# Optimization experiments

Measured on AMD Instinct MI355X. Metric: run time of the kernel, lower is better.

## Reference

```python
import jax, jax.numpy as jnp
import numpy as np
from math import log2, floor

B, N, DIM = 2, 2048, 2048
HEADS, DIM_HEAD, FF_MULT = 16, 128, 4
RMS_EPS = 1e-8


def _get_slopes(heads):
    def pow2_slopes(n):
        start = 2 ** (-2 ** (-(log2(n) - 3)))
        return [start * start ** i for i in range(n)]
    if log2(heads).is_integer():
        return pow2_slopes(heads)
    closest = 2 ** floor(log2(heads))
    return pow2_slopes(closest) + pow2_slopes(2 * closest)[0::2][: heads - closest]


def setup_inputs() -> dict:
    key = jax.random.key(0)
    ks = jax.random.split(key, 5)
    std = 0.02
    return {
        "x": jax.random.normal(ks[0], (B, N, DIM), dtype=jnp.float32),
        "g": jnp.ones((DIM,), dtype=jnp.float32),
        "w_qkv": jax.random.normal(ks[1], (DIM, DIM + DIM_HEAD), dtype=jnp.float32) * std,
        "w_attn_out": jax.random.normal(ks[2], (DIM, DIM), dtype=jnp.float32) * std,
        "w_ff1": jax.random.normal(ks[3], (DIM, 2 * FF_MULT * DIM), dtype=jnp.float32) * std,
        "w_ff2": jax.random.normal(ks[4], (FF_MULT * DIM, DIM), dtype=jnp.float32) * std,
    }


def reference(x, g, w_qkv, w_attn_out, w_ff1, w_ff2):
    b, n, dim = x.shape
    # RMSNorm: x / clamp(||x|| * dim^-0.5, eps) * g
    norm = jnp.linalg.norm(x, axis=-1, keepdims=True) * (dim ** -0.5)
    xn = x / jnp.maximum(norm, RMS_EPS) * g

    # Parallel SwiGLU FFN branch (shares normed input with attention)
    h = xn @ w_ff1                       # [b, n, 2*ff_mult*dim]
    val, gate = jnp.split(h, 2, axis=-1)
    ff_out = (jax.nn.silu(gate) * val) @ w_ff2  # [b, n, dim]

    # Multi-query attention: single dim_head-wide kv shared as K and V
    qkv = xn @ w_qkv                     # [b, n, dim + dim_head]
    q, kv = qkv[..., :dim], qkv[..., dim:]
    q = q.reshape(b, n, HEADS, DIM_HEAD) * (DIM_HEAD ** -0.5)
    sim = jnp.einsum('bihd,bjd->bhij', q, kv)  # [b, h, n, n]

    # ALiBi bias: -|j - i| * slope_h
    slopes = jnp.asarray(_get_slopes(HEADS), dtype=sim.dtype)[:, None, None]
    pos = jnp.arange(n)
    bias = -jnp.abs(pos[None, None, :] - pos[None, :, None]).astype(sim.dtype) * slopes
    sim = sim + bias

    # Causal mask (strict upper triangle masked)
    causal = jnp.triu(jnp.ones((n, n), dtype=bool), 1)
    neg = jnp.asarray(jnp.finfo(sim.dtype).max, sim.dtype)
    sim = jnp.where(causal, -neg, sim)

    attn = jax.nn.softmax(sim, axis=-1)
    out = jnp.einsum('bhij,bjd->bhid', attn, kv)     # [b, h, n, dim_head]
    out = out.transpose(0, 2, 1, 3).reshape(b, n, dim)
    return out @ w_attn_out + ff_out
```

## Files before the change

### kernel.cpp

```cpp
#include <hip/hip_runtime.h>
#include <stdint.h>

typedef unsigned short u16;
typedef __attribute__((ext_vector_type(8))) short bf16x8;
typedef __attribute__((ext_vector_type(4))) float f32x4;
typedef __attribute__((ext_vector_type(8))) unsigned short us8;
typedef __attribute__((ext_vector_type(4))) float fvec4;

#define BATCH 2
#define SEQ   2048
#define DIMM  2048
#define NH    16
#define DH    128
#define ROWS  (BATCH*SEQ)
#define QKVN  (DIMM + DH)
#define FFH   8192
#define LOG2E 1.44269504088896340736f

static __device__ __forceinline__ u16 f2bf(float x) {
  union { float f; uint32_t u; } v; v.f = x;
  uint32_t r = (v.u + 0x7fffu + ((v.u >> 16) & 1u)) >> 16;
  return (u16)r;
}

static __device__ __forceinline__ float fast_exp2(float x) {
  float r; asm("v_exp_f32 %0, %1" : "=v"(r) : "v"(x)); return r;
}

static __device__ __forceinline__ void gld_lds16(const void* g, void* l) {
  __builtin_amdgcn_global_load_lds(
      (const __attribute__((address_space(1))) uint32_t*)g,
      (__attribute__((address_space(3))) uint32_t*)l, 16, 0, 0);
}

__global__ __launch_bounds__(256)
void rmsnorm_k(const float* __restrict__ x, const float* __restrict__ g, u16* __restrict__ xn) {
  const int row = blockIdx.x;
  const float* xr = x + (size_t)row * DIMM;
  const int off = threadIdx.x * 8;
  fvec4 a = *(const fvec4*)(xr + off);
  fvec4 b = *(const fvec4*)(xr + off + 4);
  float ss = a[0]*a[0]+a[1]*a[1]+a[2]*a[2]+a[3]*a[3]
           + b[0]*b[0]+b[1]*b[1]+b[2]*b[2]+b[3]*b[3];
  #pragma unroll
  for (int m = 32; m >= 1; m >>= 1) ss += __shfl_xor(ss, m);
  __shared__ float red[4];
  if ((threadIdx.x & 63) == 0) red[threadIdx.x >> 6] = ss;
  __syncthreads();
  float tot = red[0] + red[1] + red[2] + red[3];
  float inv = 1.0f / fmaxf(sqrtf(tot * (1.0f / DIMM)), 1e-8f);
  fvec4 ga = *(const fvec4*)(g + off);
  fvec4 gb = *(const fvec4*)(g + off + 4);
  us8 o;
  #pragma unroll
  for (int i = 0; i < 4; i++) { o[i] = f2bf(a[i]*inv*ga[i]); o[4+i] = f2bf(b[i]*inv*gb[i]); }
  *(us8*)(xn + (size_t)row * DIMM + off) = o;
}

template<typename TIN>
__global__ __launch_bounds__(256)
void transpose_to_bf16(const TIN* __restrict__ in, u16* __restrict__ out, int R, int C) {
  __shared__ u16 tile[64 * 65];
  const int r0 = blockIdx.y * 64, c0 = blockIdx.x * 64;
  const int tr = threadIdx.x >> 2;
  const int tc = (threadIdx.x & 3) * 16;
  const TIN* ip = in + (size_t)(r0 + tr) * C + c0 + tc;
  u16 tmp[16];
  #pragma unroll
  for (int i = 0; i < 16; i++) {
    if constexpr (sizeof(TIN) == 4) tmp[i] = f2bf(((const float*)ip)[i]);
    else                            tmp[i] = ((const u16*)ip)[i];
  }
  #pragma unroll
  for (int i = 0; i < 16; i++) tile[tr * 65 + tc + i] = tmp[i];
  __syncthreads();
  const int oc  = c0 + tr;
  const int orr = (threadIdx.x & 3) * 16;
  us8 v0, v1;
  #pragma unroll
  for (int i = 0; i < 8; i++) v0[i] = tile[(orr + i) * 65 + tr];
  #pragma unroll
  for (int i = 0; i < 8; i++) v1[i] = tile[(orr + 8 + i) * 65 + tr];
  u16* op = out + (size_t)oc * R + r0 + orr;
  *(us8*)op = v0;
  *(us8*)(op + 8) = v1;
}

template<int MODE>
__global__ __launch_bounds__(256, 2)
void gemm_bf16(const u16* __restrict__ A, const u16* __restrict__ BT, int K,
               float* __restrict__ outF, u16* __restrict__ outQ, u16* __restrict__ outKV,
               const float* __restrict__ tmpF) {
  __shared__ __align__(16) u16 lA[128 * 32];
  __shared__ __align__(16) u16 lB[128 * 32];
  const int tid = threadIdx.x;
  const int wave = tid >> 6, lane = tid & 63;
  const int lid = lane & 15, quad = lane >> 4;
  const int wm = wave >> 1, wn = wave & 1;
  const int row0 = blockIdx.y * 128;
  const int col0 = blockIdx.x * 128;
  f32x4 acc[4][4];
  #pragma unroll
  for (int i = 0; i < 4; i++)
    #pragma unroll
    for (int j = 0; j < 4; j++) { acc[i][j][0]=0.f; acc[i][j][1]=0.f; acc[i][j][2]=0.f; acc[i][j][3]=0.f; }

  const int rA0 = wave * 32;
  const int rsub = lane >> 2;
  const int cl = lane & 3;

  for (int k0 = 0; k0 < K; k0 += 32) {
    #pragma unroll
    for (int h2 = 0; h2 < 2; ++h2) {
      int rloc = rA0 + h2 * 16 + rsub;
      int gc = cl ^ ((rloc >> 1) & 3);
      gld_lds16(A  + (size_t)(row0 + rloc) * K + k0 + gc * 8, lA + (rA0 + h2 * 16) * 32);
      gld_lds16(BT + (size_t)(col0 + rloc) * K + k0 + gc * 8, lB + (rA0 + h2 * 16) * 32);
    }
    __syncthreads();
    bf16x8 af[4], bfr[4];
    #pragma unroll
    for (int i = 0; i < 4; i++) {
      int r  = wm * 64 + i * 16 + lid;
      af[i]  = *(const bf16x8*)(lA + r * 32 + (quad ^ ((r >> 1) & 3)) * 8);
      int rb = wn * 64 + i * 16 + lid;
      bfr[i] = *(const bf16x8*)(lB + rb * 32 + (quad ^ ((rb >> 1) & 3)) * 8);
    }
    #pragma unroll
    for (int im = 0; im < 4; im++)
      #pragma unroll
      for (int in = 0; in < 4; in++)
        acc[im][in] = __builtin_amdgcn_mfma_f32_16x16x32_bf16(af[im], bfr[in], acc[im][in], 0, 0, 0);
    __syncthreads();
  }

  #pragma unroll
  for (int im = 0; im < 4; im++)
    #pragma unroll
    for (int in = 0; in < 4; in++) {
      int col = col0 + wn * 64 + in * 16 + lid;
      int rbase = row0 + wm * 64 + im * 16 + quad * 4;
      #pragma unroll
      for (int rg = 0; rg < 4; rg++) {
        float v = acc[im][in][rg];
        int row = rbase + rg;
        if constexpr (MODE == 0) {
          if (col < DIMM) outQ[(size_t)row * DIMM + col] = f2bf(v);
          else            outKV[(size_t)row * DH + (col - DIMM)] = f2bf(v);
        } else if constexpr (MODE == 2) {
          outF[(size_t)row * DIMM + col] = v;
        } else {
          size_t idx = (size_t)row * DIMM + col;
          outF[idx] += v + tmpF[idx];
        }
      }
    }
}

static __device__ __forceinline__ void stage_half(const u16* __restrict__ src, u16* dst,
                                                  int K, int sr, int sgc, int wave) {
  gld_lds16(src + (size_t)sr * K + sgc,       dst + wave * 1024);
  gld_lds16(src + (size_t)(sr + 8) * K + sgc, dst + wave * 1024 + 512);
}

static __device__ __forceinline__ void lda4(bf16x8 (&dst)[4][2], const u16* sAb,
                                            int mh, int wm, int lid, int c0) {
  #pragma unroll
  for (int i = 0; i < 4; ++i) {
    const u16* p = sAb + (mh * 128 + wm * 64 + i * 16 + lid) * 64;
    dst[i][0] = *(const bf16x8*)(p + c0);
    dst[i][1] = *(const bf16x8*)(p + (c0 ^ 32));
  }
}

static __device__ __forceinline__ void ldb2(bf16x8 (&dst)[2][2], const u16* sBb,
                                            int nh, int wn, int lid, int c0) {
  #pragma unroll
  for (int n = 0; n < 2; ++n) {
    const u16* p = sBb + (nh * 128 + wn * 32 + n * 16 + lid) * 64;
    dst[n][0] = *(const bf16x8*)(p + c0);
    dst[n][1] = *(const bf16x8*)(p + (c0 ^ 32));
  }
}

static __device__ __forceinline__ void quad16(f32x4 (&acc)[8][4], const bf16x8 (&af)[4][2],
                                              const bf16x8 (&bf)[2][2], int mh, int nh) {
  __builtin_amdgcn_s_setprio(1);
  #pragma unroll
  for (int i = 0; i < 4; ++i)
    #pragma unroll
    for (int n = 0; n < 2; ++n) {
      f32x4 c = acc[mh * 4 + i][nh * 2 + n];
      c = __builtin_amdgcn_mfma_f32_16x16x32_bf16(af[i][0], bf[n][0], c, 0, 0, 0);
      c = __builtin_amdgcn_mfma_f32_16x16x32_bf16(af[i][1], bf[n][1], c, 0, 0, 0);
      acc[mh * 4 + i][nh * 2 + n] = c;
    }
  __builtin_amdgcn_s_setprio(0);
}

#define VMW(n) asm volatile("s_waitcnt vmcnt(" #n ")" ::: "memory")
#define BAR8() __builtin_amdgcn_s_barrier()

#define EIGHT_PHASE_LOOP(NITER)                                               \
  {                                                                           \
    STAGE_A(0,0,0); STAGE_B(0,0,0); STAGE_B(0,1,0); STAGE_A(0,1,0);           \
    STAGE_A(1,0,1); STAGE_B(1,0,1); STAGE_B(1,1,1);                           \
    VMW(6);                                                                   \
    BAR8();                                                                   \
    lda4(af, sA[0], 0, wm, lid, c0);                              \
    ldb2(bW, sB[0], 0, wn, lid, c0);                              \
    for (int I = 0; I < (NITER); ++I) {                                       \
      const bool more = (I + 1 < (NITER));                                    \
      const int kt1 = 2*I+1, kt2 = 2*I+2, kt3 = 2*I+3;                        \
                                         \
      STAGE_A(1,1,kt1);                                                       \
      BAR8();                                                                 \
      quad16(acc, af, bW, 0, 0);                                              \
      ldb2(bX, sB[0], 1, wn, lid, c0);                                        \
      VMW(8);                                                                 \
      BAR8();                                                                 \
                                            \
      if (more) STAGE_A(0,0,kt2);                                             \
      BAR8();                                                                 \
      quad16(acc, af, bX, 0, 1);                                              \
      lda4(af, sA[0], 1, wm, lid, c0);                                        \
      BAR8();                                                                 \
                                                              \
      if (more) STAGE_B(0,0,kt2);                                             \
      BAR8();                                                                 \
      quad16(acc, af, bX, 1, 1);                                              \
      if (more) { VMW(8); } else { VMW(4); }                                  \
      BAR8();                                                                 \
                                    \
      if (more) STAGE_B(0,1,kt2);                                             \
      BAR8();                                                                 \
      quad16(acc, af, bW, 1, 0);                                              \
      ldb2(bW, sB[1], 0, wn, lid, c0);                                        \
      lda4(af, sA[1], 0, wm, lid, c0);                                        \
      if (more) { VMW(8); } else { VMW(2); }                                  \
      BAR8();                                                                 \
                                         \
      if (more) STAGE_A(0,1,kt2);                                             \
      BAR8();                                                                 \
      quad16(acc, af, bW, 0, 0);                                              \
      ldb2(bX, sB[1], 1, wn, lid, c0);                                        \
      if (more) { VMW(8); } else { VMW(0); }                                  \
      BAR8();                                                                 \
                                            \
      if (more) STAGE_A(1,0,kt3);                                             \
      BAR8();                                                                 \
      quad16(acc, af, bX, 0, 1);                                              \
      lda4(af, sA[1], 1, wm, lid, c0);                                        \
      BAR8();                                                                 \
                                                              \
      if (more) STAGE_B(1,0,kt3);                                             \
      BAR8();                                                                 \
      quad16(acc, af, bX, 1, 1);                                              \
      if (more) { VMW(8); }                                                   \
      BAR8();                                                                 \
                                  \
      if (more) STAGE_B(1,1,kt3);                                             \
      BAR8();                                                                 \
      quad16(acc, af, bW, 1, 0);                                              \
      if (more) {                                                             \
        ldb2(bW, sB[0], 0, wn, lid, c0);                                      \
        lda4(af, sA[0], 0, wm, lid, c0);                                      \
        VMW(8);                                                               \
      }                                                                       \
      BAR8();                                                                 \
    }                                                                         \
  }

__global__ __launch_bounds__(512, 2)
void gemm_ff1_swiglu_8p(const u16* __restrict__ A, const u16* __restrict__ BT,
                        u16* __restrict__ FF) {
  __shared__ __align__(16) u16 sA[2][256 * 64];
  __shared__ __align__(16) u16 sB[2][256 * 64];
  const int tid = threadIdx.x;
  const int wave = tid >> 6, lane = tid & 63;
  const int lid = lane & 15, quad = lane >> 4;
  const int wm = wave >> 2, wn = wave & 3;
  const int K = DIMM;

  int orig = blockIdx.y * 64 + blockIdx.x;
  int swz = (orig & 7) * 128 + (orig >> 3);
  const int row0 = (swz >> 6) * 256;
  const int n0 = (swz & 63) * 128;

  const int sr  = wave * 16 + (lane >> 3);
  const int sgc = (((lane & 7) ^ (lane >> 3)) << 3);
  const int c0  = ((quad ^ (lid & 7)) << 3);

  f32x4 acc[8][4];
  #pragma unroll
  for (int i = 0; i < 8; ++i)
    #pragma unroll
    for (int j = 0; j < 4; ++j) { acc[i][j][0]=0.f; acc[i][j][1]=0.f; acc[i][j][2]=0.f; acc[i][j][3]=0.f; }
  bf16x8 af[4][2], bW[2][2], bX[2][2];

  #define STAGE_A(b, h, kt) stage_half(A  + (size_t)(row0 + (h)*128) * K + (kt)*64, &sA[b][(h)*8192], K, sr, sgc, wave)
  #define STAGE_B(b, h, kt) stage_half(BT + (size_t)((h) ? (FFH + n0) : n0) * K + (kt)*64, &sB[b][(h)*8192], K, sr, sgc, wave)

  EIGHT_PHASE_LOOP(K / 128)

  #undef STAGE_A
  #undef STAGE_B

  #pragma unroll
  for (int mi = 0; mi < 8; ++mi) {
    const int row = row0 + (mi >> 2) * 128 + wm * 64 + (mi & 3) * 16 + quad * 4;
    #pragma unroll
    for (int n = 0; n < 2; ++n) {
      const int col = n0 + wn * 32 + n * 16 + lid;
      #pragma unroll
      for (int rg = 0; rg < 4; ++rg) {
        float vv = acc[mi][n][rg];
        float gg = acc[mi][2 + n][rg];
        float sig = 1.0f / (1.0f + fast_exp2(-gg * LOG2E));
        FF[(size_t)(row + rg) * FFH + col] = f2bf(vv * gg * sig);
      }
    }
  }
}

__global__ __launch_bounds__(512, 2)
void gemm_ff2_8p(const u16* __restrict__ A, const u16* __restrict__ BT,
                 float* __restrict__ out0, float* __restrict__ out1) {
  __shared__ __align__(16) u16 sA[2][256 * 64];
  __shared__ __align__(16) u16 sB[2][256 * 64];
  const int tid = threadIdx.x;
  const int wave = tid >> 6, lane = tid & 63;
  const int lid = lane & 15, quad = lane >> 4;
  const int wm = wave >> 2, wn = wave & 3;
  const int K = FFH;

  int orig = (blockIdx.z * 16 + blockIdx.y) * 8 + blockIdx.x;
  int swz = (orig & 7) * 32 + (orig >> 3);
  const int n0   = (swz & 7) * 256;
  const int ks   = (swz >> 3) & 1;
  const int row0 = (swz >> 4) * 256;

  const u16* Ab = A  + ks * 4096;
  const u16* Bb = BT + ks * 4096;

  const int sr  = wave * 16 + (lane >> 3);
  const int sgc = (((lane & 7) ^ (lane >> 3)) << 3);
  const int c0  = ((quad ^ (lid & 7)) << 3);

  f32x4 acc[8][4];
  #pragma unroll
  for (int i = 0; i < 8; ++i)
    #pragma unroll
    for (int j = 0; j < 4; ++j) { acc[i][j][0]=0.f; acc[i][j][1]=0.f; acc[i][j][2]=0.f; acc[i][j][3]=0.f; }
  bf16x8 af[4][2], bW[2][2], bX[2][2];

  #define STAGE_A(b, h, kt) stage_half(Ab + (size_t)(row0 + (h)*128) * K + (kt)*64, &sA[b][(h)*8192], K, sr, sgc, wave)
  #define STAGE_B(b, h, kt) stage_half(Bb + (size_t)(n0 + (h)*128) * K + (kt)*64,  &sB[b][(h)*8192], K, sr, sgc, wave)

  EIGHT_PHASE_LOOP(32)

  #undef STAGE_A
  #undef STAGE_B

  float* dst = ks ? out1 : out0;
  #pragma unroll
  for (int mi = 0; mi < 8; ++mi) {
    const int row = row0 + (mi >> 2) * 128 + wm * 64 + (mi & 3) * 16 + quad * 4;
    #pragma unroll
    for (int j = 0; j < 4; ++j) {
      const int col = n0 + (j >> 1) * 128 + wn * 32 + (j & 1) * 16 + lid;
      #pragma unroll
      for (int rg = 0; rg < 4; ++rg)
        dst[(size_t)(row + rg) * DIMM + col] = acc[mi][j][rg];
    }
  }
}

__global__ __launch_bounds__(256, 1)
void attn_k2(const u16* __restrict__ qws, const u16* __restrict__ kvws,
             const u16* __restrict__ kvt, u16* __restrict__ attnws) {
  __shared__ __align__(16) u16 kvls[128 * 128];
  __shared__ __align__(16) u16 kvtls[128 * 128];
  __shared__ __align__(16) u16 plds[4][32][136];
  const int tid = threadIdx.x;
  const int wave = tid >> 6, lane = tid & 63;
  const int lid = lane & 15, quad = lane >> 4;
  const int hb = blockIdx.y;
  const int h = hb & (NH - 1), b = hb >> 4;
  const int pair = blockIdx.x;
  const float slope2 = fast_exp2(-0.5f * (float)(h + 1)) * LOG2E;
  const float scale2 = 0.08838834764831845f * LOG2E;
  const float NEG = -__builtin_inff();

  const u16* kvb  = kvws + (size_t)b * SEQ * DH;
  const u16* kvtb = kvt  + (size_t)b * DH * SEQ;

  #pragma unroll 1
  for (int tt = 0; tt < 2; tt++) {
    const int T = tt ? (15 - pair) : pair;
    const int rw = T * 128 + wave * 32;

    bf16x8 qf[2][4];
    #pragma unroll
    for (int ig = 0; ig < 2; ig++)
      #pragma unroll
      for (int ks = 0; ks < 4; ks++)
        qf[ig][ks] = *(const bf16x8*)(qws + (size_t)(b * SEQ + rw + ig * 16 + lid) * DIMM
                                       + h * DH + ks * 32 + quad * 8);
    float srow2[2][4];
    #pragma unroll
    for (int ig = 0; ig < 2; ig++)
      #pragma unroll
      for (int rg = 0; rg < 4; rg++)
        srow2[ig][rg] = slope2 * (float)(rw + ig * 16 + quad * 4 + rg);

    f32x4 o[2][8];
    #pragma unroll
    for (int ig = 0; ig < 2; ig++)
      #pragma unroll
      for (int nd = 0; nd < 8; nd++) { o[ig][nd][0]=0.f; o[ig][nd][1]=0.f; o[ig][nd][2]=0.f; o[ig][nd][3]=0.f; }
    float m2[2][4], l[2][4];
    #pragma unroll
    for (int ig = 0; ig < 2; ig++)
      #pragma unroll
      for (int rg = 0; rg < 4; rg++) { m2[ig][rg] = NEG; l[ig][rg] = 0.f; }

    const int njt = T + 1;
    #pragma unroll 1
    for (int jt = 0; jt < njt; jt++) {
      const int j0 = jt * 128;
      __syncthreads();
      {
        const int c = lane & 15;
        const int r4 = lane >> 4;
        #pragma unroll
        for (int it = 0; it < 8; it++) {
          const int r = wave * 32 + it * 4 + r4;
          const int gc = c ^ (r & 15);
          gld_lds16(kvb  + (size_t)(j0 + r) * DH + gc * 8,        kvls  + (wave * 32 + it * 4) * 128);
          gld_lds16(kvtb + (size_t)r * SEQ + j0 + gc * 8,         kvtls + (wave * 32 + it * 4) * 128);
        }
      }
      __syncthreads();

      const int rhi = rw + 31;
      const int nbmax = min(8, ((rhi - j0) >> 4) + 1);
      const int ks2max = (nbmax + 1) >> 1;

      float pvv[2][8][4];
      float mt[2][4];
      #pragma unroll
      for (int ig = 0; ig < 2; ig++)
        #pragma unroll
        for (int rg = 0; rg < 4; rg++) mt[ig][rg] = NEG;

      #pragma unroll
      for (int nb = 0; nb < 8; nb++) {
        if (nb < nbmax) {
          bf16x8 bk[4];
          #pragma unroll
          for (int ks = 0; ks < 4; ks++)
            bk[ks] = *(const bf16x8*)(kvls + (nb * 16 + lid) * 128 + (((ks * 4 + quad) ^ lid) << 3));
          f32x4 s0, s1;
          s0[0]=0.f;s0[1]=0.f;s0[2]=0.f;s0[3]=0.f;
          s1[0]=0.f;s1[1]=0.f;s1[2]=0.f;s1[3]=0.f;
          #pragma unroll
          for (int ks = 0; ks < 4; ks++) {
            s0 = __builtin_amdgcn_mfma_f32_16x16x32_bf16(qf[0][ks], bk[ks], s0, 0, 0, 0);
            s1 = __builtin_amdgcn_mfma_f32_16x16x32_bf16(qf[1][ks], bk[ks], s1, 0, 0, 0);
          }
          const int jl = j0 + nb * 16 + lid;
          const float sj = slope2 * (float)jl;
          #pragma unroll
          for (int rg = 0; rg < 4; rg++) {
            const int row0r = rw + quad * 4 + rg;
            float e0 = fmaf(s0[rg], scale2, sj) - srow2[0][rg];
            e0 = (jl <= row0r) ? e0 : NEG;
            pvv[0][nb][rg] = e0;
            mt[0][rg] = fmaxf(mt[0][rg], e0);
            float e1 = fmaf(s1[rg], scale2, sj) - srow2[1][rg];
            e1 = (jl <= row0r + 16) ? e1 : NEG;
            pvv[1][nb][rg] = e1;
            mt[1][rg] = fmaxf(mt[1][rg], e1);
          }
        }
      }

      float alpha[2][4];
      #pragma unroll
      for (int ig = 0; ig < 2; ig++)
        #pragma unroll
        for (int rg = 0; rg < 4; rg++) {
          float m = mt[ig][rg];
          m = fmaxf(m, __shfl_xor(m, 1));
          m = fmaxf(m, __shfl_xor(m, 2));
          m = fmaxf(m, __shfl_xor(m, 4));
          m = fmaxf(m, __shfl_xor(m, 8));
          float mn = fmaxf(m2[ig][rg], m);
          alpha[ig][rg] = fast_exp2(m2[ig][rg] - mn);
          m2[ig][rg] = mn;
        }

      float rs[2][4];
      #pragma unroll
      for (int ig = 0; ig < 2; ig++)
        #pragma unroll
        for (int rg = 0; rg < 4; rg++) rs[ig][rg] = 0.f;
      #pragma unroll
      for (int nb = 0; nb < 8; nb++) {
        if (nb < nbmax) {
          #pragma unroll
          for (int ig = 0; ig < 2; ig++)
            #pragma unroll
            for (int rg = 0; rg < 4; rg++) {
              float p = fast_exp2(pvv[ig][nb][rg] - m2[ig][rg]);
              rs[ig][rg] += p;
              plds[wave][ig * 16 + quad * 4 + rg][nb * 16 + lid] = f2bf(p);
            }
        }
      }
      if (nbmax & 1) {
        #pragma unroll
        for (int ig = 0; ig < 2; ig++)
          #pragma unroll
          for (int rg = 0; rg < 4; rg++)
            plds[wave][ig * 16 + quad * 4 + rg][nbmax * 16 + lid] = 0;
      }

      #pragma unroll
      for (int ig = 0; ig < 2; ig++)
        #pragma unroll
        for (int rg = 0; rg < 4; rg++) {
          float r = rs[ig][rg];
          r += __shfl_xor(r, 1);
          r += __shfl_xor(r, 2);
          r += __shfl_xor(r, 4);
          r += __shfl_xor(r, 8);
          l[ig][rg] = l[ig][rg] * alpha[ig][rg] + r;
        }
      #pragma unroll
      for (int ig = 0; ig < 2; ig++)
        #pragma unroll
        for (int nd = 0; nd < 8; nd++)
          #pragma unroll
          for (int rg = 0; rg < 4; rg++) o[ig][nd][rg] *= alpha[ig][rg];

      asm volatile("s_waitcnt lgkmcnt(0)" ::: "memory");
      #pragma unroll
      for (int ks2 = 0; ks2 < 4; ks2++) {
        if (ks2 < ks2max) {
          bf16x8 pa0 = *(const bf16x8*)&plds[wave][lid][ks2 * 32 + quad * 8];
          bf16x8 pa1 = *(const bf16x8*)&plds[wave][16 + lid][ks2 * 32 + quad * 8];
          #pragma unroll
          for (int nd = 0; nd < 8; nd++) {
            bf16x8 bv = *(const bf16x8*)(kvtls + (nd * 16 + lid) * 128 + (((ks2 * 4 + quad) ^ lid) << 3));
            o[0][nd] = __builtin_amdgcn_mfma_f32_16x16x32_bf16(pa0, bv, o[0][nd], 0, 0, 0);
            o[1][nd] = __builtin_amdgcn_mfma_f32_16x16x32_bf16(pa1, bv, o[1][nd], 0, 0, 0);
          }
        }
      }
    }

    #pragma unroll
    for (int ig = 0; ig < 2; ig++) {
      float inv[4];
      #pragma unroll
      for (int rg = 0; rg < 4; rg++) inv[rg] = 1.0f / l[ig][rg];
      #pragma unroll
      for (int nd = 0; nd < 8; nd++)
        #pragma unroll
        for (int rg = 0; rg < 4; rg++) {
          int row = rw + ig * 16 + quad * 4 + rg;
          attnws[(size_t)(b * SEQ + row) * DIMM + h * DH + nd * 16 + lid] =
              f2bf(o[ig][nd][rg] * inv[rg]);
        }
    }
  }
}

extern "C" void kernel_launch(void* const* d_in, const int* in_sizes, int n_in,
                              void* d_out, int out_size, void* d_ws, size_t ws_size,
                              hipStream_t stream) {
  (void)in_sizes; (void)n_in; (void)out_size; (void)ws_size;
  const float* x     = (const float*)d_in[0];
  const float* g     = (const float*)d_in[1];
  const float* w_qkv = (const float*)d_in[2];
  const float* w_ao  = (const float*)d_in[3];
  const float* w_ff1 = (const float*)d_in[4];
  const float* w_ff2 = (const float*)d_in[5];
  float* out = (float*)d_out;

  u16* ws = (u16*)d_ws;
  u16* xn     = ws;
  u16* wTqkv  = xn     + 8388608;
  u16* wTattn = wTqkv  + 4456448;
  u16* wTff1  = wTattn + 4194304;
  u16* wTff2  = wTff1  + 33554432;
  u16* ffin   = wTff2  + 16777216;
  u16* qws    = ffin   + 33554432;
  u16* kvws   = qws    + 8388608;
  u16* kvtws  = kvws   + 524288;
  u16* attnws = kvtws  + 524288;
  float* tmpf = (float*)wTff1;

  transpose_to_bf16<float><<<dim3(QKVN/64, DIMM/64), 256, 0, stream>>>(w_qkv, wTqkv, DIMM, QKVN);
  transpose_to_bf16<float><<<dim3(DIMM/64, DIMM/64), 256, 0, stream>>>(w_ao, wTattn, DIMM, DIMM);
  transpose_to_bf16<float><<<dim3((2*FFH)/64, DIMM/64), 256, 0, stream>>>(w_ff1, wTff1, DIMM, 2*FFH);
  transpose_to_bf16<float><<<dim3(DIMM/64, FFH/64), 256, 0, stream>>>(w_ff2, wTff2, FFH, DIMM);

  rmsnorm_k<<<ROWS, 256, 0, stream>>>(x, g, xn);

  gemm_bf16<0><<<dim3(QKVN/128, ROWS/128), 256, 0, stream>>>(xn, wTqkv, DIMM, nullptr, qws, kvws, nullptr);

  transpose_to_bf16<u16><<<dim3(DH/64, SEQ/64), 256, 0, stream>>>(kvws, kvtws, SEQ, DH);
  transpose_to_bf16<u16><<<dim3(DH/64, SEQ/64), 256, 0, stream>>>(kvws + (size_t)SEQ*DH, kvtws + (size_t)DH*SEQ, SEQ, DH);

  attn_k2<<<dim3(8, NH*BATCH), 256, 0, stream>>>(qws, kvws, kvtws, attnws);

  gemm_ff1_swiglu_8p<<<dim3(FFH/128, ROWS/256), 512, 0, stream>>>(xn, wTff1, ffin);
  gemm_ff2_8p<<<dim3(8, 16, 2), 512, 0, stream>>>(ffin, wTff2, out, tmpf);

  gemm_bf16<3><<<dim3(DIMM/128, ROWS/128), 256, 0, stream>>>(attnws, wTattn, DIMM, out, nullptr, nullptr, tmpf);
}
```

Before: 924.6 us.

## Shrink attention tiles to 64 rows and double grid for higher occupancy

Reworks the flash-attention kernel to process 64 query rows per block (16 per wave) against 64-column KV tiles, halving LDS use and allowing two blocks per CU. The grid doubles so more blocks cover the GPU and latency can be hidden across blocks. In exchange each wave reuses loaded K fragments across fewer MFMAs, KV tiles are reloaded from global memory twice as often, and block-level syncs per unit of work increase.

```diff
diff --git a/kernel.cpp b/kernel.cpp
--- a/kernel.cpp
+++ b/kernel.cpp
@@ -376,12 +376,12 @@
   }
 }
 
-__global__ __launch_bounds__(256, 1)
-void attn_k2(const u16* __restrict__ qws, const u16* __restrict__ kvws,
+__global__ __launch_bounds__(256, 2)
+void attn_k3(const u16* __restrict__ qws, const u16* __restrict__ kvws,
              const u16* __restrict__ kvt, u16* __restrict__ attnws) {
-  __shared__ __align__(16) u16 kvls[128 * 128];
-  __shared__ __align__(16) u16 kvtls[128 * 128];
-  __shared__ __align__(16) u16 plds[4][32][136];
+  __shared__ __align__(16) u16 kvls[64 * 128];
+  __shared__ __align__(16) u16 kvtls[128 * 64];
+  __shared__ __align__(16) u16 plds[4][16][72];
   const int tid = threadIdx.x;
   const int wave = tid >> 6, lane = tid & 63;
   const int lid = lane & 15, quad = lane >> 4;
@@ -397,184 +397,152 @@
 
   #pragma unroll 1
   for (int tt = 0; tt < 2; tt++) {
-    const int T = tt ? (15 - pair) : pair;
-    const int rw = T * 128 + wave * 32;
-
-    bf16x8 qf[2][4];
-    #pragma unroll
-    for (int ig = 0; ig < 2; ig++)
-      #pragma unroll
-      for (int ks = 0; ks < 4; ks++)
-        qf[ig][ks] = *(const bf16x8*)(qws + (size_t)(b * SEQ + rw + ig * 16 + lid) * DIMM
-                                       + h * DH + ks * 32 + quad * 8);
-    float srow2[2][4];
-    #pragma unroll
-    for (int ig = 0; ig < 2; ig++)
-      #pragma unroll
-      for (int rg = 0; rg < 4; rg++)
-        srow2[ig][rg] = slope2 * (float)(rw + ig * 16 + quad * 4 + rg);
-
-    f32x4 o[2][8];
-    #pragma unroll
-    for (int ig = 0; ig < 2; ig++)
-      #pragma unroll
-      for (int nd = 0; nd < 8; nd++) { o[ig][nd][0]=0.f; o[ig][nd][1]=0.f; o[ig][nd][2]=0.f; o[ig][nd][3]=0.f; }
-    float m2[2][4], l[2][4];
-    #pragma unroll
-    for (int ig = 0; ig < 2; ig++)
-      #pragma unroll
-      for (int rg = 0; rg < 4; rg++) { m2[ig][rg] = NEG; l[ig][rg] = 0.f; }
-
-    const int njt = T + 1;
+    const int TT = tt ? (31 - pair) : pair;
+    const int rw = TT * 64 + wave * 16;
+
+    bf16x8 qf[4];
+    #pragma unroll
+    for (int ks = 0; ks < 4; ks++)
+      qf[ks] = *(const bf16x8*)(qws + (size_t)(b * SEQ + rw + lid) * DIMM
+                                 + h * DH + ks * 32 + quad * 8);
+    float srow[4];
+    #pragma unroll
+    for (int rg = 0; rg < 4; rg++)
+      srow[rg] = slope2 * (float)(rw + quad * 4 + rg);
+
+    f32x4 o[8];
+    #pragma unroll
+    for (int nd = 0; nd < 8; nd++) { o[nd][0]=0.f; o[nd][1]=0.f; o[nd][2]=0.f; o[nd][3]=0.f; }
+    float m2[4], l[4];
+    #pragma unroll
+    for (int rg = 0; rg < 4; rg++) { m2[rg] = NEG; l[rg] = 0.f; }
+
+    const int njt = TT + 1;
     #pragma unroll 1
     for (int jt = 0; jt < njt; jt++) {
-      const int j0 = jt * 128;
+      const int j0 = jt * 64;
       __syncthreads();
       {
-        const int c = lane & 15;
-        const int r4 = lane >> 4;
+        const int c16 = lane & 15, r16 = lane >> 4;
+        const int c8  = lane & 7,  r8  = lane >> 3;
         #pragma unroll
-        for (int it = 0; it < 8; it++) {
-          const int r = wave * 32 + it * 4 + r4;
-          const int gc = c ^ (r & 15);
-          gld_lds16(kvb  + (size_t)(j0 + r) * DH + gc * 8,        kvls  + (wave * 32 + it * 4) * 128);
-          gld_lds16(kvtb + (size_t)r * SEQ + j0 + gc * 8,         kvtls + (wave * 32 + it * 4) * 128);
+        for (int it = 0; it < 4; it++) {
+          const int r  = wave * 16 + it * 4 + r16;
+          const int gc = c16 ^ (r & 15);
+          gld_lds16(kvb + (size_t)(j0 + r) * DH + gc * 8, kvls + (wave * 16 + it * 4) * 128);
+          const int r2  = wave * 32 + it * 8 + r8;
+          const int gc2 = c8 ^ (r2 & 7);
+          gld_lds16(kvtb + (size_t)r2 * SEQ + j0 + gc2 * 8, kvtls + (wave * 32 + it * 8) * 64);
         }
       }
       __syncthreads();
 
-      const int rhi = rw + 31;
-      const int nbmax = min(8, ((rhi - j0) >> 4) + 1);
+      const int nbmax = min(4, ((rw + 15 - j0) >> 4) + 1);
       const int ks2max = (nbmax + 1) >> 1;
 
-      float pvv[2][8][4];
-      float mt[2][4];
-      #pragma unroll
-      for (int ig = 0; ig < 2; ig++)
-        #pragma unroll
-        for (int rg = 0; rg < 4; rg++) mt[ig][rg] = NEG;
-
-      #pragma unroll
-      for (int nb = 0; nb < 8; nb++) {
+      float pvv[4][4];
+      float mt[4];
+      #pragma unroll
+      for (int rg = 0; rg < 4; rg++) mt[rg] = NEG;
+
+      #pragma unroll
+      for (int nb = 0; nb < 4; nb++) {
         if (nb < nbmax) {
           bf16x8 bk[4];
           #pragma unroll
           for (int ks = 0; ks < 4; ks++)
             bk[ks] = *(const bf16x8*)(kvls + (nb * 16 + lid) * 128 + (((ks * 4 + quad) ^ lid) << 3));
-          f32x4 s0, s1;
-          s0[0]=0.f;s0[1]=0.f;s0[2]=0.f;s0[3]=0.f;
-          s1[0]=0.f;s1[1]=0.f;s1[2]=0.f;s1[3]=0.f;
+          f32x4 s;
+          s[0]=0.f; s[1]=0.f; s[2]=0.f; s[3]=0.f;
           #pragma unroll
-          for (int ks = 0; ks < 4; ks++) {
-            s0 = __builtin_amdgcn_mfma_f32_16x16x32_bf16(qf[0][ks], bk[ks], s0, 0, 0, 0);
-            s1 = __builtin_amdgcn_mfma_f32_16x16x32_bf16(qf[1][ks], bk[ks], s1, 0, 0, 0);
-          }
+          for (int ks = 0; ks < 4; ks++)
+            s = __builtin_amdgcn_mfma_f32_16x16x32_bf16(qf[ks], bk[ks], s, 0, 0, 0);
           const int jl = j0 + nb * 16 + lid;
           const float sj = slope2 * (float)jl;
           #pragma unroll
           for (int rg = 0; rg < 4; rg++) {
             const int row0r = rw + quad * 4 + rg;
-            float e0 = fmaf(s0[rg], scale2, sj) - srow2[0][rg];
-            e0 = (jl <= row0r) ? e0 : NEG;
-            pvv[0][nb][rg] = e0;
-            mt[0][rg] = fmaxf(mt[0][rg], e0);
-            float e1 = fmaf(s1[rg], scale2, sj) - srow2[1][rg];
-            e1 = (jl <= row0r + 16) ? e1 : NEG;
-            pvv[1][nb][rg] = e1;
-            mt[1][rg] = fmaxf(mt[1][rg], e1);
+            float e = fmaf(s[rg], scale2, sj) - srow[rg];
+            e = (jl <= row0r) ? e : NEG;
+            pvv[nb][rg] = e;
+            mt[rg] = fmaxf(mt[rg], e);
           }
         }
       }
 
-      float alpha[2][4];
-      #pragma unroll
-      for (int ig = 0; ig < 2; ig++)
-        #pragma unroll
-        for (int rg = 0; rg < 4; rg++) {
-          float m = mt[ig][rg];
-          m = fmaxf(m, __shfl_xor(m, 1));
-          m = fmaxf(m, __shfl_xor(m, 2));
-          m = fmaxf(m, __shfl_xor(m, 4));
-          m = fmaxf(m, __shfl_xor(m, 8));
-          float mn = fmaxf(m2[ig][rg], m);
-          alpha[ig][rg] = fast_exp2(m2[ig][rg] - mn);
-          m2[ig][rg] = mn;
-        }
-
-      float rs[2][4];
-      #pragma unroll
-      for (int ig = 0; ig < 2; ig++)
-        #pragma unroll
-        for (int rg = 0; rg < 4; rg++) rs[ig][rg] = 0.f;
-      #pragma unroll
-      for (int nb = 0; nb < 8; nb++) {
+      float alpha[4];
+      #pragma unroll
+      for (int rg = 0; rg < 4; rg++) {
+        float m = mt[rg];
+        m = fmaxf(m, __shfl_xor(m, 1));
+        m = fmaxf(m, __shfl_xor(m, 2));
+        m = fmaxf(m, __shfl_xor(m, 4));
+        m = fmaxf(m, __shfl_xor(m, 8));
+        float mn = fmaxf(m2[rg], m);
+        alpha[rg] = fast_exp2(m2[rg] - mn);
+        m2[rg] = mn;
+      }
+
+      float rs[4];
+      #pragma unroll
+      for (int rg = 0; rg < 4; rg++) rs[rg] = 0.f;
+      #pragma unroll
+      for (int nb = 0; nb < 4; nb++) {
         if (nb < nbmax) {
           #pragma unroll
-          for (int ig = 0; ig < 2; ig++)
-            #pragma unroll
-            for (int rg = 0; rg < 4; rg++) {
-              float p = fast_exp2(pvv[ig][nb][rg] - m2[ig][rg]);
-              rs[ig][rg] += p;
-              plds[wave][ig * 16 + quad * 4 + rg][nb * 16 + lid] = f2bf(p);
-            }
+          for (int rg = 0; rg < 4; rg++) {
+            float p = fast_exp2(pvv[nb][rg] - m2[rg]);
+            rs[rg] += p;
+            plds[wave][quad * 4 + rg][nb * 16 + lid] = f2bf(p);
+          }
         }
       }
       if (nbmax & 1) {
         #pragma unroll
-        for (int ig = 0; ig < 2; ig++)
-          #pragma unroll
-          for (int rg = 0; rg < 4; rg++)
-            plds[wave][ig * 16 + quad * 4 + rg][nbmax * 16 + lid] = 0;
-      }
-
-      #pragma unroll
-      for (int ig = 0; ig < 2; ig++)
+        for (int rg = 0; rg < 4; rg++)
+          plds[wave][quad * 4 + rg][nbmax * 16 + lid] = 0;
+      }
+
+      #pragma unroll
+      for (int rg = 0; rg < 4; rg++) {
+        float r = rs[rg];
+        r += __shfl_xor(r, 1);
+        r += __shfl_xor(r, 2);
+        r += __shfl_xor(r, 4);
+        r += __shfl_xor(r, 8);
+        l[rg] = l[rg] * alpha[rg] + r;
+      }
+      #pragma unroll
+      for (int nd = 0; nd < 8; nd++)
         #pragma unroll
-        for (int rg = 0; rg < 4; rg++) {
-          float r = rs[ig][rg];
-          r += __shfl_xor(r, 1);
-          r += __shfl_xor(r, 2);
-          r += __shfl_xor(r, 4);
-          r += __shfl_xor(r, 8);
-          l[ig][rg] = l[ig][rg] * alpha[ig][rg] + r;
-        }
-      #pragma unroll
-      for (int ig = 0; ig < 2; ig++)
-        #pragma unroll
-        for (int nd = 0; nd < 8; nd++)
-          #pragma unroll
-          for (int rg = 0; rg < 4; rg++) o[ig][nd][rg] *= alpha[ig][rg];
+        for (int rg = 0; rg < 4; rg++) o[nd][rg] *= alpha[rg];
 
       asm volatile("s_waitcnt lgkmcnt(0)" ::: "memory");
       #pragma unroll
-      for (int ks2 = 0; ks2 < 4; ks2++) {
+      for (int ks2 = 0; ks2 < 2; ks2++) {
         if (ks2 < ks2max) {
-          bf16x8 pa0 = *(const bf16x8*)&plds[wave][lid][ks2 * 32 + quad * 8];
-          bf16x8 pa1 = *(const bf16x8*)&plds[wave][16 + lid][ks2 * 32 + quad * 8];
+          bf16x8 pa = *(const bf16x8*)&plds[wave][lid][ks2 * 32 + quad * 8];
           #pragma unroll
           for (int nd = 0; nd < 8; nd++) {
-            bf16x8 bv = *(const bf16x8*)(kvtls + (nd * 16 + lid) * 128 + (((ks2 * 4 + quad) ^ lid) << 3));
-            o[0][nd] = __builtin_amdgcn_mfma_f32_16x16x32_bf16(pa0, bv, o[0][nd], 0, 0, 0);
-            o[1][nd] = __builtin_amdgcn_mfma_f32_16x16x32_bf16(pa1, bv, o[1][nd], 0, 0, 0);
+            bf16x8 bv = *(const bf16x8*)(kvtls + (nd * 16 + lid) * 64
+                                          + (((ks2 * 4 + quad) ^ (lid & 7)) << 3));
+            o[nd] = __builtin_amdgcn_mfma_f32_16x16x32_bf16(pa, bv, o[nd], 0, 0, 0);
           }
         }
       }
     }
 
-    #pragma unroll
-    for (int ig = 0; ig < 2; ig++) {
-      float inv[4];
-      #pragma unroll
-      for (int rg = 0; rg < 4; rg++) inv[rg] = 1.0f / l[ig][rg];
-      #pragma unroll
-      for (int nd = 0; nd < 8; nd++)
-        #pragma unroll
-        for (int rg = 0; rg < 4; rg++) {
-          int row = rw + ig * 16 + quad * 4 + rg;
-          attnws[(size_t)(b * SEQ + row) * DIMM + h * DH + nd * 16 + lid] =
-              f2bf(o[ig][nd][rg] * inv[rg]);
-        }
-    }
+    float inv[4];
+    #pragma unroll
+    for (int rg = 0; rg < 4; rg++) inv[rg] = 1.0f / l[rg];
+    #pragma unroll
+    for (int nd = 0; nd < 8; nd++)
+      #pragma unroll
+      for (int rg = 0; rg < 4; rg++) {
+        int row = rw + quad * 4 + rg;
+        attnws[(size_t)(b * SEQ + row) * DIMM + h * DH + nd * 16 + lid] =
+            f2bf(o[nd][rg] * inv[rg]);
+      }
   }
 }
 
@@ -615,7 +583,7 @@
   transpose_to_bf16<u16><<<dim3(DH/64, SEQ/64), 256, 0, stream>>>(kvws, kvtws, SEQ, DH);
   transpose_to_bf16<u16><<<dim3(DH/64, SEQ/64), 256, 0, stream>>>(kvws + (size_t)SEQ*DH, kvtws + (size_t)DH*SEQ, SEQ, DH);
 
-  attn_k2<<<dim3(8, NH*BATCH), 256, 0, stream>>>(qws, kvws, kvtws, attnws);
+  attn_k3<<<dim3(16, NH*BATCH), 256, 0, stream>>>(qws, kvws, kvtws, attnws);
 
   gemm_ff1_swiglu_8p<<<dim3(FFH/128, ROWS/256), 512, 0, stream>>>(xn, wTff1, ffin);
   gemm_ff2_8p<<<dim3(8, 16, 2), 512, 0, stream>>>(ffin, wTff2, out, tmpf);
```

Result: no change. 908.0 us (-1.8%).
